# Performance work log

Measured on AMD Instinct MI355X. Metric: run time of the kernel, lower is better.

Reference implementation:

```python
import jax, jax.numpy as jnp
import numpy as np

T, D, F, E, K, R = 16384, 1024, 2048, 8, 2, 16
LORA_SCALING = 2.0


def setup_inputs() -> dict:
    key = jax.random.key(0)
    ks = jax.random.split(key, 9)
    s = 0.02
    return {
        "hidden_states": jax.random.normal(ks[0], (T, D), jnp.float32),
        "gate_weight": jax.random.normal(ks[1], (E, D), jnp.float32) * s,
        "gate_lora_delta": jax.random.normal(ks[2], (E, D), jnp.float32) * s,
        "gate_up_proj": jax.random.normal(ks[3], (E, D, 2 * F), jnp.float32) * s,
        "down_proj": jax.random.normal(ks[4], (E, F, D), jnp.float32) * s,
        "gu_lora_A": jax.random.normal(ks[5], (E, R, D), jnp.float32) * s,
        "gu_lora_B": jax.random.normal(ks[6], (E, 2 * F, R), jnp.float32) * s,
        "dn_lora_A": jax.random.normal(ks[7], (E, R, F), jnp.float32) * s,
        "dn_lora_B": jax.random.normal(ks[8], (E, D, R), jnp.float32) * s,
    }


def reference(hidden_states, gate_weight, gate_lora_delta, gate_up_proj,
              down_proj, gu_lora_A, gu_lora_B, dn_lora_A, dn_lora_B):
    x = hidden_states  # [T, D]
    # --- softmax top-k routing (base gate weight + LoRA delta) ---
    logits = x @ gate_weight.T + x @ gate_lora_delta.T            # [T, E]
    probs = jax.nn.softmax(logits.astype(jnp.float32), axis=-1)   # fp32 softmax
    topk_w, topk_idx = jax.lax.top_k(probs, K)                    # [T, K]
    topk_w = topk_w / jnp.sum(topk_w, axis=-1, keepdims=True)     # norm_topk_prob
    # dense combine weights [T, E]: 0 for unselected experts
    combine = jnp.zeros((x.shape[0], E), jnp.float32)
    combine = combine.at[jnp.arange(x.shape[0])[:, None], topk_idx].set(topk_w)
    # --- per-expert gated MLP with LoRA deltas, masked combine ---
    out = jnp.zeros_like(x, dtype=jnp.float32)
    for e in range(E):  # fixed small expert count
        gu = x @ gate_up_proj[e] + LORA_SCALING * ((x @ gu_lora_A[e].T) @ gu_lora_B[e].T)  # [T, 2F]
        gate, up = jnp.split(gu, 2, axis=-1)
        h = jax.nn.silu(gate) * up                                                        # [T, F]
        y = h @ down_proj[e] + LORA_SCALING * ((h @ dn_lora_A[e].T) @ dn_lora_B[e].T)     # [T, D]
        out = out + combine[:, e:e + 1] * y
    return out.astype(hidden_states.dtype)
```

## Files before the change

kernel.cpp:

```cpp
#include <hip/hip_runtime.h>
#include <stdint.h>

#define T_TOK 16384
#define DH    1024
#define FF    2048
#define NE    8
#define NC    4096
#define PADROWS 33792

typedef __attribute__((ext_vector_type(8))) __bf16 bf16x8;
typedef __attribute__((ext_vector_type(4))) float  f32x4;

__device__ __forceinline__ float bf2f(unsigned short s) {
  unsigned int u = ((unsigned int)s) << 16;
  return __builtin_bit_cast(float, u);
}
__device__ __forceinline__ unsigned short f2bf(float f) {
  unsigned int u = __builtin_bit_cast(unsigned int, f);
  u += 0x7fffu + ((u >> 16) & 1u);
  return (unsigned short)(u >> 16);
}

__device__ __forceinline__ void gload_lds16(const void* g, void* l) {
  __builtin_amdgcn_global_load_lds(
      (__attribute__((address_space(1))) void*)(uintptr_t)g,
      (__attribute__((address_space(3))) void*)(uint32_t)(uintptr_t)l,
      16, 0, 0);
}

__device__ __forceinline__ int origc_gu(int c) {
  int g = c >> 5, wi = c & 31;
  return ((wi >> 4) << 11) | (g * 16 + (wi & 15));
}

__global__ __launch_bounds__(256) void fold_gu_kernel(
    const float* __restrict__ Wg,
    const float* __restrict__ A,
    const float* __restrict__ B,
    unsigned short* __restrict__ Wf)
{
  const int e = blockIdx.x, d0 = blockIdx.y * 64, c0 = blockIdx.z * 64;
  __shared__ float tile[64][65];
  __shared__ float Al[16][64];
  __shared__ float Bl[64][17];
  const int tid = threadIdx.x;
  {
    int r = tid >> 4, dc = (tid & 15) * 4;
    float4 v = *(const float4*)&A[((size_t)e * 16 + r) * DH + d0 + dc];
    Al[r][dc] = v.x; Al[r][dc + 1] = v.y; Al[r][dc + 2] = v.z; Al[r][dc + 3] = v.w;
  }
  {
    int c = tid >> 2, rr = (tid & 3) * 4;
    float4 v = *(const float4*)&B[((size_t)e * NC + origc_gu(c0 + c)) * 16 + rr];
    Bl[c][rr] = v.x; Bl[c][rr + 1] = v.y; Bl[c][rr + 2] = v.z; Bl[c][rr + 3] = v.w;
  }
  __syncthreads();
  const int d = tid >> 2;
  const int cq0 = (tid & 3) * 4;
  float areg[16];
#pragma unroll
  for (int r = 0; r < 16; r++) areg[r] = Al[r][d];
#pragma unroll
  for (int p = 0; p < 4; p++) {
    const int cq = p * 16 + cq0;
    float4 v = *(const float4*)&Wg[((size_t)e * DH + d0 + d) * NC + origc_gu(c0 + cq)];
    float s0 = 0.f, s1 = 0.f, s2 = 0.f, s3 = 0.f;
#pragma unroll
    for (int r = 0; r < 16; r++) {
      float a = areg[r];
      s0 += a * Bl[cq][r];     s1 += a * Bl[cq + 1][r];
      s2 += a * Bl[cq + 2][r]; s3 += a * Bl[cq + 3][r];
    }
    tile[d][cq]     = v.x + 2.f * s0; tile[d][cq + 1] = v.y + 2.f * s1;
    tile[d][cq + 2] = v.z + 2.f * s2; tile[d][cq + 3] = v.w + 2.f * s3;
  }
  __syncthreads();
#pragma unroll
  for (int p = 0; p < 2; p++) {
    int flat = p * 256 + tid;
    int c = flat >> 3, dch = (flat & 7) * 8;
    unsigned short u[8];
#pragma unroll
    for (int j = 0; j < 8; j++) u[j] = f2bf(tile[dch + j][c]);
    *(uint4*)&Wf[((size_t)e * NC + c0 + c) * DH + d0 + dch] = *(uint4*)u;
  }
}

__global__ __launch_bounds__(256) void fold_dn_kernel(
    const float* __restrict__ Wd,
    const float* __restrict__ A,
    const float* __restrict__ B,
    unsigned short* __restrict__ Wf)
{
  const int e = blockIdx.x, f0 = blockIdx.y * 64, d0 = blockIdx.z * 64;
  __shared__ float tile[64][65];
  __shared__ float Al[16][64];
  __shared__ float Bl[64][17];
  const int tid = threadIdx.x;
  {
    int r = tid >> 4, fc = (tid & 15) * 4;
    float4 v = *(const float4*)&A[((size_t)e * 16 + r) * FF + f0 + fc];
    Al[r][fc] = v.x; Al[r][fc + 1] = v.y; Al[r][fc + 2] = v.z; Al[r][fc + 3] = v.w;
  }
  {
    int d = tid >> 2, rr = (tid & 3) * 4;
    float4 v = *(const float4*)&B[((size_t)e * DH + d0 + d) * 16 + rr];
    Bl[d][rr] = v.x; Bl[d][rr + 1] = v.y; Bl[d][rr + 2] = v.z; Bl[d][rr + 3] = v.w;
  }
  __syncthreads();
  const int f = tid >> 2;
  const int dq0 = (tid & 3) * 4;
  float areg[16];
#pragma unroll
  for (int r = 0; r < 16; r++) areg[r] = Al[r][f];
#pragma unroll
  for (int p = 0; p < 4; p++) {
    const int dq = p * 16 + dq0;
    float4 v = *(const float4*)&Wd[((size_t)e * FF + f0 + f) * DH + d0 + dq];
    float s0 = 0.f, s1 = 0.f, s2 = 0.f, s3 = 0.f;
#pragma unroll
    for (int r = 0; r < 16; r++) {
      float a = areg[r];
      s0 += a * Bl[dq][r];     s1 += a * Bl[dq + 1][r];
      s2 += a * Bl[dq + 2][r]; s3 += a * Bl[dq + 3][r];
    }
    tile[f][dq]     = v.x + 2.f * s0; tile[f][dq + 1] = v.y + 2.f * s1;
    tile[f][dq + 2] = v.z + 2.f * s2; tile[f][dq + 3] = v.w + 2.f * s3;
  }
  __syncthreads();
#pragma unroll
  for (int p = 0; p < 2; p++) {
    int flat = p * 256 + tid;
    int d = flat >> 3, fch = (flat & 7) * 8;
    unsigned short u[8];
#pragma unroll
    for (int j = 0; j < 8; j++) u[j] = f2bf(tile[fch + j][d]);
    *(uint4*)&Wf[((size_t)e * DH + d0 + d) * FF + f0 + fch] = *(uint4*)u;
  }
}

__global__ __launch_bounds__(256) void route_kernel(
    const float* __restrict__ X,
    const float* __restrict__ GW,
    const float* __restrict__ GLD,
    unsigned short* __restrict__ Xbf,
    int* __restrict__ tokE, float* __restrict__ tokW, int* __restrict__ counts)
{
  __shared__ float gc[NE * DH];
  __shared__ int bc[NE];
  const int tid = threadIdx.x;
  if (tid < NE) bc[tid] = 0;
  for (int i = tid; i < NE * DH; i += 256) gc[i] = GW[i] + GLD[i];
  __syncthreads();
  const int w = tid >> 6, lane = tid & 63;
  for (int it = 0; it < 8; it++) {
    const int t = blockIdx.x * 32 + w * 8 + it;
    float s[NE];
#pragma unroll
    for (int e = 0; e < NE; e++) s[e] = 0.f;
#pragma unroll
    for (int i = 0; i < 8; i++) {
      const int base = 2 * lane + 128 * i;
      const float2 xv = *(const float2*)&X[(size_t)t * DH + base];
      *(unsigned*)&Xbf[(size_t)t * DH + base] =
          (unsigned)f2bf(xv.x) | ((unsigned)f2bf(xv.y) << 16);
#pragma unroll
      for (int e = 0; e < NE; e++) {
        float2 g2 = *(const float2*)&gc[e * DH + base];
        s[e] += xv.x * g2.x + xv.y * g2.y;
      }
    }
#pragma unroll
    for (int e = 0; e < NE; e++) {
#pragma unroll
      for (int off = 32; off > 0; off >>= 1) s[e] += __shfl_xor(s[e], off);
    }
    int e1 = 0; float l1 = s[0];
#pragma unroll
    for (int e = 1; e < NE; e++) { if (s[e] > l1) { l1 = s[e]; e1 = e; } }
    int e2i = 0; float l2 = -3.4e38f;
#pragma unroll
    for (int e = 0; e < NE; e++) { if (e != e1 && s[e] > l2) { l2 = s[e]; e2i = e; } }
    float r = __expf(l2 - l1);
    float w0 = 1.f / (1.f + r);
    if (lane == 0) {
      tokE[2 * t] = e1; tokE[2 * t + 1] = e2i;
      tokW[2 * t] = w0; tokW[2 * t + 1] = 1.f - w0;
      atomicAdd(&bc[e1], 1); atomicAdd(&bc[e2i], 1);
    }
  }
  __syncthreads();
  if (tid < NE) atomicAdd(&counts[tid], bc[tid]);
}

__global__ void offs_kernel(const int* __restrict__ counts, int* __restrict__ offs) {
  if (threadIdx.x == 0) {
    int run = 0;
#pragma unroll
    for (int e = 0; e < NE; e++) { offs[e] = run; run += (counts[e] + 127) & ~127; }
    offs[NE] = run;
  }
}

__global__ void scatter_kernel(const int* __restrict__ tokE,
                               const int* __restrict__ offs,
                               int* __restrict__ cursor,
                               int* __restrict__ posTok,
                               int* __restrict__ posOf)
{
  const int t = blockIdx.x * 256 + threadIdx.x;
  const int lane = threadIdx.x & 63;
#pragma unroll
  for (int k = 0; k < 2; k++) {
    const int e = tokE[2 * t + k];
    int p = 0;
#pragma unroll
    for (int ei = 0; ei < NE; ei++) {
      unsigned long long mask = __ballot(e == ei);
      if (mask) {
        int leader = __ffsll((unsigned long long)mask) - 1;
        int base = 0;
        if (lane == leader) base = atomicAdd(&cursor[ei], (int)__popcll(mask));
        base = __shfl(base, leader);
        if (e == ei)
          p = offs[ei] + base + (int)__popcll(mask & ((1ull << lane) - 1ull));
      }
    }
    if (p < 0) p = 0;
    if (p >= PADROWS) p = PADROWS - 1;
    posTok[p] = t;
    posOf[2 * t + k] = p;
  }
}

__global__ __launch_bounds__(256) void gemm1_kernel(
    const unsigned short* __restrict__ Xbf,
    const unsigned short* __restrict__ Wgu,
    const int* __restrict__ posTok,
    const int* __restrict__ offs,
    unsigned short* __restrict__ H)
{
  __shared__ __align__(16) unsigned short As[128 * 32];
  __shared__ __align__(16) unsigned short Bs[128 * 32];
  const int n0 = blockIdx.x * 128;
  const int row0 = blockIdx.y * 128;
  if (row0 >= offs[NE]) return;
  int e = 0;
#pragma unroll
  for (int i = 1; i < NE; i++) e += (row0 >= offs[i]) ? 1 : 0;
  const unsigned short* Wb = Wgu + (size_t)e * NC * DH;

  const int tid = threadIdx.x;
  const int lane = tid & 63;
  const int w = tid >> 6;
  const int wm = w >> 1, wn = w & 1;
  const int l15 = lane & 15, quad = lane >> 4;

  const int srow  = tid >> 2;
  const int skoff = (tid & 3) * 8;
  int t0 = posTok[row0 + srow];      if (t0 < 0) t0 = 0;
  int t1 = posTok[row0 + 64 + srow]; if (t1 < 0) t1 = 0;
  const unsigned short* gA0 = Xbf + (size_t)t0 * DH + skoff;
  const unsigned short* gA1 = Xbf + (size_t)t1 * DH + skoff;
  const unsigned short* gB0 = Wb + (size_t)(n0 + srow) * DH + skoff;
  const unsigned short* gB1 = Wb + (size_t)(n0 + 64 + srow) * DH + skoff;
  unsigned short* lA0 = As + (w * 64) * 8;
  unsigned short* lA1 = As + (256 + w * 64) * 8;
  unsigned short* lB0 = Bs + (w * 64) * 8;
  unsigned short* lB1 = Bs + (256 + w * 64) * 8;

  const unsigned short* Ard = As + (size_t)(wm * 64 + l15) * 32 + quad * 8;
  const unsigned short* Brd = Bs + (size_t)(wn * 64 + l15) * 32 + quad * 8;

  f32x4 acc[4][4];
#pragma unroll
  for (int mi = 0; mi < 4; mi++)
#pragma unroll
    for (int ni = 0; ni < 4; ni++) acc[mi][ni] = (f32x4){0.f, 0.f, 0.f, 0.f};

  for (int k0 = 0; k0 < DH; k0 += 32) {
    gload_lds16(gA0, lA0);
    gload_lds16(gA1, lA1);
    gload_lds16(gB0, lB0);
    gload_lds16(gB1, lB1);
    gA0 += 32; gA1 += 32; gB0 += 32; gB1 += 32;
    __syncthreads();
    bf16x8 af[4], bv[4];
#pragma unroll
    for (int mi = 0; mi < 4; mi++) af[mi] = *(const bf16x8*)(Ard + mi * 16 * 32);
#pragma unroll
    for (int ni = 0; ni < 4; ni++) bv[ni] = *(const bf16x8*)(Brd + ni * 16 * 32);
#pragma unroll
    for (int mi = 0; mi < 4; mi++)
#pragma unroll
      for (int ni = 0; ni < 4; ni++)
        acc[mi][ni] = __builtin_amdgcn_mfma_f32_16x16x32_bf16(af[mi], bv[ni], acc[mi][ni], 0, 0, 0);
    __syncthreads();
  }

  const int rowb = row0 + wm * 64;
#pragma unroll
  for (int mi = 0; mi < 4; mi++) {
#pragma unroll
    for (int p = 0; p < 2; p++) {
      f32x4 g = acc[mi][2 * p], u = acc[mi][2 * p + 1];
      int f = (n0 >> 1) + wn * 32 + p * 16 + l15;
#pragma unroll
      for (int r = 0; r < 4; r++) {
        int row = rowb + mi * 16 + quad * 4 + r;
        float gv = g[r];
        float hv = (gv / (1.f + __expf(-gv))) * u[r];
        H[(size_t)row * FF + f] = f2bf(hv);
      }
    }
  }
}

__global__ __launch_bounds__(256) void gemm2_kernel(
    const unsigned short* __restrict__ H,
    const unsigned short* __restrict__ Wdn,
    const int* __restrict__ offs,
    unsigned short* __restrict__ Y)
{
  __shared__ __align__(16) unsigned short As[128 * 32];
  __shared__ __align__(16) unsigned short Bs[128 * 32];
  const int n0 = blockIdx.x * 128;
  const int row0 = blockIdx.y * 128;
  if (row0 >= offs[NE]) return;
  int e = 0;
#pragma unroll
  for (int i = 1; i < NE; i++) e += (row0 >= offs[i]) ? 1 : 0;
  const unsigned short* Wb = Wdn + (size_t)e * DH * FF;

  const int tid = threadIdx.x;
  const int lane = tid & 63;
  const int w = tid >> 6;
  const int wm = w >> 1, wn = w & 1;
  const int l15 = lane & 15, quad = lane >> 4;

  const int srow  = tid >> 2;
  const int skoff = (tid & 3) * 8;
  const unsigned short* gA0 = H + (size_t)(row0 + srow) * FF + skoff;
  const unsigned short* gA1 = H + (size_t)(row0 + 64 + srow) * FF + skoff;
  const unsigned short* gB0 = Wb + (size_t)(n0 + srow) * FF + skoff;
  const unsigned short* gB1 = Wb + (size_t)(n0 + 64 + srow) * FF + skoff;
  unsigned short* lA0 = As + (w * 64) * 8;
  unsigned short* lA1 = As + (256 + w * 64) * 8;
  unsigned short* lB0 = Bs + (w * 64) * 8;
  unsigned short* lB1 = Bs + (256 + w * 64) * 8;

  const unsigned short* Ard = As + (size_t)(wm * 64 + l15) * 32 + quad * 8;
  const unsigned short* Brd = Bs + (size_t)(wn * 64 + l15) * 32 + quad * 8;

  f32x4 acc[4][4];
#pragma unroll
  for (int mi = 0; mi < 4; mi++)
#pragma unroll
    for (int ni = 0; ni < 4; ni++) acc[mi][ni] = (f32x4){0.f, 0.f, 0.f, 0.f};

  for (int k0 = 0; k0 < FF; k0 += 32) {
    gload_lds16(gA0, lA0);
    gload_lds16(gA1, lA1);
    gload_lds16(gB0, lB0);
    gload_lds16(gB1, lB1);
    gA0 += 32; gA1 += 32; gB0 += 32; gB1 += 32;
    __syncthreads();
    bf16x8 af[4], bv[4];
#pragma unroll
    for (int mi = 0; mi < 4; mi++) af[mi] = *(const bf16x8*)(Ard + mi * 16 * 32);
#pragma unroll
    for (int ni = 0; ni < 4; ni++) bv[ni] = *(const bf16x8*)(Brd + ni * 16 * 32);
#pragma unroll
    for (int mi = 0; mi < 4; mi++)
#pragma unroll
      for (int ni = 0; ni < 4; ni++)
        acc[mi][ni] = __builtin_amdgcn_mfma_f32_16x16x32_bf16(af[mi], bv[ni], acc[mi][ni], 0, 0, 0);
    __syncthreads();
  }

#pragma unroll
  for (int mi = 0; mi < 4; mi++)
#pragma unroll
    for (int ni = 0; ni < 4; ni++) {
      int col = n0 + wn * 64 + ni * 16 + l15;
#pragma unroll
      for (int r = 0; r < 4; r++) {
        int row = row0 + wm * 64 + mi * 16 + quad * 4 + r;
        Y[(size_t)row * DH + col] = f2bf(acc[mi][ni][r]);
      }
    }
}

__global__ void combine_kernel(const unsigned short* __restrict__ Y,
                               const int* __restrict__ posOf,
                               const float* __restrict__ tokW,
                               float* __restrict__ out)
{
  int idx = blockIdx.x * 256 + threadIdx.x;
  int t = idx >> 7;
  int c = (idx & 127) * 8;
  int p0 = posOf[2 * t], p1 = posOf[2 * t + 1];
  float w0 = tokW[2 * t], w1 = tokW[2 * t + 1];
  const uint4 a = *(const uint4*)&Y[(size_t)p0 * DH + c];
  const uint4 b = *(const uint4*)&Y[(size_t)p1 * DH + c];
  const unsigned* ap = (const unsigned*)&a;
  const unsigned* bp = (const unsigned*)&b;
  float4 o0, o1;
#pragma unroll
  for (int i = 0; i < 4; i++) {
    float a0 = bf2f((unsigned short)(ap[i] & 0xffff)), a1 = bf2f((unsigned short)(ap[i] >> 16));
    float b0 = bf2f((unsigned short)(bp[i] & 0xffff)), b1 = bf2f((unsigned short)(bp[i] >> 16));
    float r0 = w0 * a0 + w1 * b0;
    float r1 = w0 * a1 + w1 * b1;
    if (i < 2) { ((float*)&o0)[2 * i] = r0; ((float*)&o0)[2 * i + 1] = r1; }
    else       { ((float*)&o1)[2 * (i - 2)] = r0; ((float*)&o1)[2 * (i - 2) + 1] = r1; }
  }
  *(float4*)&out[(size_t)t * DH + c]     = o0;
  *(float4*)&out[(size_t)t * DH + c + 4] = o1;
}

extern "C" void kernel_launch(void* const* d_in, const int* in_sizes, int n_in,
                              void* d_out, int out_size, void* d_ws, size_t ws_size,
                              hipStream_t stream)
{
  const float* X   = (const float*)d_in[0];
  const float* GW  = (const float*)d_in[1];
  const float* GLD = (const float*)d_in[2];
  const float* GUP = (const float*)d_in[3];
  const float* DNP = (const float*)d_in[4];
  const float* GUA = (const float*)d_in[5];
  const float* GUB = (const float*)d_in[6];
  const float* DNA = (const float*)d_in[7];
  const float* DNB = (const float*)d_in[8];
  float* OUT = (float*)d_out;

  char* p = (char*)d_ws;
  unsigned short* Wguf = (unsigned short*)p; p += (size_t)NE * NC * DH * 2;
  unsigned short* Wdnf = (unsigned short*)p; p += (size_t)NE * DH * FF * 2;
  unsigned short* H    = (unsigned short*)p; p += (size_t)PADROWS * FF * 2;
  unsigned short* Y    = (unsigned short*)p; p += (size_t)PADROWS * DH * 2;
  int*   posTok = (int*)p;   p += (size_t)PADROWS * 4;
  int*   posOf  = (int*)p;   p += (size_t)T_TOK * 2 * 4;
  int*   tokE   = (int*)p;   p += (size_t)T_TOK * 2 * 4;
  float* tokW   = (float*)p; p += (size_t)T_TOK * 2 * 4;
  int*   counts = (int*)p;   p += 32;
  int*   cursor = (int*)p;   p += 32;
  int*   offs   = (int*)p;   p += 64;
  if ((size_t)(p - (char*)d_ws) > ws_size) return;

  unsigned short* Xbf = Y;

  hipMemsetAsync(counts, 0, 32 + 32 + 64, stream);
  hipMemsetAsync(posTok, 0xFF, (size_t)PADROWS * 4, stream);

  fold_gu_kernel<<<dim3(NE, DH / 64, NC / 64), 256, 0, stream>>>(GUP, GUA, GUB, Wguf);
  fold_dn_kernel<<<dim3(NE, FF / 64, DH / 64), 256, 0, stream>>>(DNP, DNA, DNB, Wdnf);
  route_kernel<<<T_TOK / 32, 256, 0, stream>>>(X, GW, GLD, Xbf, tokE, tokW, counts);
  offs_kernel<<<1, 64, 0, stream>>>(counts, offs);
  scatter_kernel<<<T_TOK / 256, 256, 0, stream>>>(tokE, offs, cursor, posTok, posOf);
  gemm1_kernel<<<dim3(NC / 128, PADROWS / 128), 256, 0, stream>>>(Xbf, Wguf, posTok, offs, H);
  gemm2_kernel<<<dim3(DH / 128, PADROWS / 128), 256, 0, stream>>>(H, Wdnf, offs, Y);
  combine_kernel<<<(T_TOK * DH / 8) / 256, 256, 0, stream>>>(Y, posOf, tokW, OUT);
}
```

Before: 943.9 us.

## Use 256x256 tiles with 4-stage LDS pipeline and swizzled layout in expert GEMMs

Both grouped GEMMs now use 256x256 output tiles with 512 threads (8 waves, each computing 128x64), padding expert segments to 256 rows. Global-to-LDS loads run in a 4-deep ring, issued three k-steps ahead with explicit vmcnt waits, and the MFMA work is split into two phases separated by barriers and raised wave priority. An XOR swizzle on LDS chunk placement is meant to reduce bank conflicts on fragment reads. The aim is to hide memory latency and raise arithmetic intensity, at the cost of more padding waste, higher register and LDS use, and fewer blocks in flight.

```diff
diff --git a/kernel.cpp b/kernel.cpp
--- a/kernel.cpp
+++ b/kernel.cpp
@@ -6,7 +6,8 @@
 #define FF    2048
 #define NE    8
 #define NC    4096
-#define PADROWS 33792
+#define PADROWS 34816
+#define BK    32
 
 typedef __attribute__((ext_vector_type(8))) __bf16 bf16x8;
 typedef __attribute__((ext_vector_type(4))) float  f32x4;
@@ -34,10 +35,8 @@
 }
 
 __global__ __launch_bounds__(256) void fold_gu_kernel(
-    const float* __restrict__ Wg,
-    const float* __restrict__ A,
-    const float* __restrict__ B,
-    unsigned short* __restrict__ Wf)
+    const float* __restrict__ Wg, const float* __restrict__ A,
+    const float* __restrict__ B, unsigned short* __restrict__ Wf)
 {
   const int e = blockIdx.x, d0 = blockIdx.y * 64, c0 = blockIdx.z * 64;
   __shared__ float tile[64][65];
@@ -87,10 +86,8 @@
 }
 
 __global__ __launch_bounds__(256) void fold_dn_kernel(
-    const float* __restrict__ Wd,
-    const float* __restrict__ A,
-    const float* __restrict__ B,
-    unsigned short* __restrict__ Wf)
+    const float* __restrict__ Wd, const float* __restrict__ A,
+    const float* __restrict__ B, unsigned short* __restrict__ Wf)
 {
   const int e = blockIdx.x, f0 = blockIdx.y * 64, d0 = blockIdx.z * 64;
   __shared__ float tile[64][65];
@@ -197,7 +194,7 @@
   if (threadIdx.x == 0) {
     int run = 0;
 #pragma unroll
-    for (int e = 0; e < NE; e++) { offs[e] = run; run += (counts[e] + 127) & ~127; }
+    for (int e = 0; e < NE; e++) { offs[e] = run; run += (counts[e] + 255) & ~255; }
     offs[NE] = run;
   }
 }
@@ -233,17 +230,35 @@
   }
 }
 
-__global__ __launch_bounds__(256) void gemm1_kernel(
+
+#define STAGE_A(s) { unsigned short* d_ = (unsigned short*)&lds[(s) & 3][0][w * 512]; \
+  gload_lds16(gA0 + (size_t)(s) * BK, d_); gload_lds16(gA1 + (size_t)(s) * BK, d_ + 4096); }
+#define STAGE_B(s) { unsigned short* d_ = (unsigned short*)&lds[(s) & 3][1][w * 512]; \
+  gload_lds16(gB0 + (size_t)(s) * BK, d_); gload_lds16(gB1 + (size_t)(s) * BK, d_ + 4096); }
+
+#define PHASE_MFMA(ACCROW, AV)                                              \
+  __builtin_amdgcn_s_barrier();                                             \
+  __builtin_amdgcn_s_setprio(1);                                            \
+  _Pragma("unroll")                                                         \
+  for (int mi = 0; mi < 4; mi++)                                            \
+    _Pragma("unroll")                                                       \
+    for (int ni = 0; ni < 4; ni++)                                          \
+      acc[(ACCROW) + mi][ni] = __builtin_amdgcn_mfma_f32_16x16x32_bf16(     \
+          AV[mi], b[ni], acc[(ACCROW) + mi][ni], 0, 0, 0);                  \
+  __builtin_amdgcn_s_setprio(0);                                            \
+  __builtin_amdgcn_s_barrier();
+
+__global__ __launch_bounds__(512, 2) void gemm1_kernel(
     const unsigned short* __restrict__ Xbf,
     const unsigned short* __restrict__ Wgu,
     const int* __restrict__ posTok,
     const int* __restrict__ offs,
     unsigned short* __restrict__ H)
 {
-  __shared__ __align__(16) unsigned short As[128 * 32];
-  __shared__ __align__(16) unsigned short Bs[128 * 32];
-  const int n0 = blockIdx.x * 128;
-  const int row0 = blockIdx.y * 128;
+  __shared__ __align__(16) unsigned short lds[4][2][8192];
+  const int NT = DH / BK;
+  const int n0 = blockIdx.x * 256;
+  const int row0 = blockIdx.y * 256;
   if (row0 >= offs[NE]) return;
   int e = 0;
 #pragma unroll
@@ -253,54 +268,57 @@
   const int tid = threadIdx.x;
   const int lane = tid & 63;
   const int w = tid >> 6;
-  const int wm = w >> 1, wn = w & 1;
+  const int wm = w >> 2, wn = w & 3;
   const int l15 = lane & 15, quad = lane >> 4;
 
-  const int srow  = tid >> 2;
-  const int skoff = (tid & 3) * 8;
-  int t0 = posTok[row0 + srow];      if (t0 < 0) t0 = 0;
-  int t1 = posTok[row0 + 64 + srow]; if (t1 < 0) t1 = 0;
-  const unsigned short* gA0 = Xbf + (size_t)t0 * DH + skoff;
-  const unsigned short* gA1 = Xbf + (size_t)t1 * DH + skoff;
-  const unsigned short* gB0 = Wb + (size_t)(n0 + srow) * DH + skoff;
-  const unsigned short* gB1 = Wb + (size_t)(n0 + 64 + srow) * DH + skoff;
-  unsigned short* lA0 = As + (w * 64) * 8;
-  unsigned short* lA1 = As + (256 + w * 64) * 8;
-  unsigned short* lB0 = Bs + (w * 64) * 8;
-  unsigned short* lB1 = Bs + (256 + w * 64) * 8;
-
-  const unsigned short* Ard = As + (size_t)(wm * 64 + l15) * 32 + quad * 8;
-  const unsigned short* Brd = Bs + (size_t)(wn * 64 + l15) * 32 + quad * 8;
-
-  f32x4 acc[4][4];
-#pragma unroll
-  for (int mi = 0; mi < 4; mi++)
+  const int srow = tid >> 2;
+  const int sch  = (tid & 3) ^ ((srow >> 1) & 3);
+  int t0 = posTok[row0 + srow];       if (t0 < 0) t0 = 0;
+  int t1 = posTok[row0 + 128 + srow]; if (t1 < 0) t1 = 0;
+  const unsigned short* gA0 = Xbf + (size_t)t0 * DH + sch * 8;
+  const unsigned short* gA1 = Xbf + (size_t)t1 * DH + sch * 8;
+  const unsigned short* gB0 = Wb + (size_t)(n0 + srow) * DH + sch * 8;
+  const unsigned short* gB1 = Wb + (size_t)(n0 + 128 + srow) * DH + sch * 8;
+
+  const int slot  = quad ^ ((l15 >> 1) & 3);
+  const int aBase = (wm * 128 + l15) * 32 + slot * 8;
+  const int bBase = (wn * 64 + l15) * 32 + slot * 8;
+
+  f32x4 acc[8][4];
+#pragma unroll
+  for (int mi = 0; mi < 8; mi++)
 #pragma unroll
     for (int ni = 0; ni < 4; ni++) acc[mi][ni] = (f32x4){0.f, 0.f, 0.f, 0.f};
 
-  for (int k0 = 0; k0 < DH; k0 += 32) {
-    gload_lds16(gA0, lA0);
-    gload_lds16(gA1, lA1);
-    gload_lds16(gB0, lB0);
-    gload_lds16(gB1, lB1);
-    gA0 += 32; gA1 += 32; gB0 += 32; gB1 += 32;
-    __syncthreads();
-    bf16x8 af[4], bv[4];
-#pragma unroll
-    for (int mi = 0; mi < 4; mi++) af[mi] = *(const bf16x8*)(Ard + mi * 16 * 32);
-#pragma unroll
-    for (int ni = 0; ni < 4; ni++) bv[ni] = *(const bf16x8*)(Brd + ni * 16 * 32);
-#pragma unroll
-    for (int mi = 0; mi < 4; mi++)
-#pragma unroll
-      for (int ni = 0; ni < 4; ni++)
-        acc[mi][ni] = __builtin_amdgcn_mfma_f32_16x16x32_bf16(af[mi], bv[ni], acc[mi][ni], 0, 0, 0);
-    __syncthreads();
-  }
-
-  const int rowb = row0 + wm * 64;
-#pragma unroll
-  for (int mi = 0; mi < 4; mi++) {
+  STAGE_A(0); STAGE_B(0);
+  STAGE_A(1); STAGE_B(1);
+  STAGE_A(2); STAGE_B(2);
+  asm volatile("s_waitcnt vmcnt(8)" ::: "memory");
+  __builtin_amdgcn_s_barrier();
+
+  for (int kt = 0; kt < NT; ++kt) {
+    const unsigned short* LA = &lds[kt & 3][0][0];
+    const unsigned short* LB = &lds[kt & 3][1][0];
+    bf16x8 a[4], b[4];
+#pragma unroll
+    for (int i = 0; i < 4; i++) a[i] = *(const bf16x8*)&LA[aBase + i * 512];
+#pragma unroll
+    for (int i = 0; i < 4; i++) b[i] = *(const bf16x8*)&LB[bBase + i * 512];
+    if (kt + 3 < NT) STAGE_A(kt + 3);
+    PHASE_MFMA(0, a)
+    bf16x8 a2[4];
+#pragma unroll
+    for (int i = 0; i < 4; i++) a2[i] = *(const bf16x8*)&LA[aBase + (4 + i) * 512];
+    if (kt + 3 < NT) STAGE_B(kt + 3);
+    if (kt + 3 < NT)       { asm volatile("s_waitcnt vmcnt(8)" ::: "memory"); }
+    else if (kt + 3 == NT) { asm volatile("s_waitcnt vmcnt(4)" ::: "memory"); }
+    else if (kt + 1 < NT)  { asm volatile("s_waitcnt vmcnt(0)" ::: "memory"); }
+    PHASE_MFMA(4, a2)
+  }
+
+  const int rowb = row0 + wm * 128;
+#pragma unroll
+  for (int mi = 0; mi < 8; mi++) {
 #pragma unroll
     for (int p = 0; p < 2; p++) {
       f32x4 g = acc[mi][2 * p], u = acc[mi][2 * p + 1];
@@ -316,16 +334,16 @@
   }
 }
 
-__global__ __launch_bounds__(256) void gemm2_kernel(
+__global__ __launch_bounds__(512, 2) void gemm2_kernel(
     const unsigned short* __restrict__ H,
     const unsigned short* __restrict__ Wdn,
     const int* __restrict__ offs,
     unsigned short* __restrict__ Y)
 {
-  __shared__ __align__(16) unsigned short As[128 * 32];
-  __shared__ __align__(16) unsigned short Bs[128 * 32];
-  const int n0 = blockIdx.x * 128;
-  const int row0 = blockIdx.y * 128;
+  __shared__ __align__(16) unsigned short lds[4][2][8192];
+  const int NT = FF / BK;
+  const int n0 = blockIdx.x * 256;
+  const int row0 = blockIdx.y * 256;
   if (row0 >= offs[NE]) return;
   int e = 0;
 #pragma unroll
@@ -335,57 +353,60 @@
   const int tid = threadIdx.x;
   const int lane = tid & 63;
   const int w = tid >> 6;
-  const int wm = w >> 1, wn = w & 1;
+  const int wm = w >> 2, wn = w & 3;
   const int l15 = lane & 15, quad = lane >> 4;
 
-  const int srow  = tid >> 2;
-  const int skoff = (tid & 3) * 8;
-  const unsigned short* gA0 = H + (size_t)(row0 + srow) * FF + skoff;
-  const unsigned short* gA1 = H + (size_t)(row0 + 64 + srow) * FF + skoff;
-  const unsigned short* gB0 = Wb + (size_t)(n0 + srow) * FF + skoff;
-  const unsigned short* gB1 = Wb + (size_t)(n0 + 64 + srow) * FF + skoff;
-  unsigned short* lA0 = As + (w * 64) * 8;
-  unsigned short* lA1 = As + (256 + w * 64) * 8;
-  unsigned short* lB0 = Bs + (w * 64) * 8;
-  unsigned short* lB1 = Bs + (256 + w * 64) * 8;
-
-  const unsigned short* Ard = As + (size_t)(wm * 64 + l15) * 32 + quad * 8;
-  const unsigned short* Brd = Bs + (size_t)(wn * 64 + l15) * 32 + quad * 8;
-
-  f32x4 acc[4][4];
-#pragma unroll
-  for (int mi = 0; mi < 4; mi++)
+  const int srow = tid >> 2;
+  const int sch  = (tid & 3) ^ ((srow >> 1) & 3);
+  const unsigned short* gA0 = H + (size_t)(row0 + srow) * FF + sch * 8;
+  const unsigned short* gA1 = H + (size_t)(row0 + 128 + srow) * FF + sch * 8;
+  const unsigned short* gB0 = Wb + (size_t)(n0 + srow) * FF + sch * 8;
+  const unsigned short* gB1 = Wb + (size_t)(n0 + 128 + srow) * FF + sch * 8;
+
+  const int slot  = quad ^ ((l15 >> 1) & 3);
+  const int aBase = (wm * 128 + l15) * 32 + slot * 8;
+  const int bBase = (wn * 64 + l15) * 32 + slot * 8;
+
+  f32x4 acc[8][4];
+#pragma unroll
+  for (int mi = 0; mi < 8; mi++)
 #pragma unroll
     for (int ni = 0; ni < 4; ni++) acc[mi][ni] = (f32x4){0.f, 0.f, 0.f, 0.f};
 
-  for (int k0 = 0; k0 < FF; k0 += 32) {
-    gload_lds16(gA0, lA0);
-    gload_lds16(gA1, lA1);
-    gload_lds16(gB0, lB0);
-    gload_lds16(gB1, lB1);
-    gA0 += 32; gA1 += 32; gB0 += 32; gB1 += 32;
-    __syncthreads();
-    bf16x8 af[4], bv[4];
-#pragma unroll
-    for (int mi = 0; mi < 4; mi++) af[mi] = *(const bf16x8*)(Ard + mi * 16 * 32);
-#pragma unroll
-    for (int ni = 0; ni < 4; ni++) bv[ni] = *(const bf16x8*)(Brd + ni * 16 * 32);
-#pragma unroll
-    for (int mi = 0; mi < 4; mi++)
-#pragma unroll
-      for (int ni = 0; ni < 4; ni++)
-        acc[mi][ni] = __builtin_amdgcn_mfma_f32_16x16x32_bf16(af[mi], bv[ni], acc[mi][ni], 0, 0, 0);
-    __syncthreads();
-  }
-
-#pragma unroll
-  for (int mi = 0; mi < 4; mi++)
+  STAGE_A(0); STAGE_B(0);
+  STAGE_A(1); STAGE_B(1);
+  STAGE_A(2); STAGE_B(2);
+  asm volatile("s_waitcnt vmcnt(8)" ::: "memory");
+  __builtin_amdgcn_s_barrier();
+
+  for (int kt = 0; kt < NT; ++kt) {
+    const unsigned short* LA = &lds[kt & 3][0][0];
+    const unsigned short* LB = &lds[kt & 3][1][0];
+    bf16x8 a[4], b[4];
+#pragma unroll
+    for (int i = 0; i < 4; i++) a[i] = *(const bf16x8*)&LA[aBase + i * 512];
+#pragma unroll
+    for (int i = 0; i < 4; i++) b[i] = *(const bf16x8*)&LB[bBase + i * 512];
+    if (kt + 3 < NT) STAGE_A(kt + 3);
+    PHASE_MFMA(0, a)
+    bf16x8 a2[4];
+#pragma unroll
+    for (int i = 0; i < 4; i++) a2[i] = *(const bf16x8*)&LA[aBase + (4 + i) * 512];
+    if (kt + 3 < NT) STAGE_B(kt + 3);
+    if (kt + 3 < NT)       { asm volatile("s_waitcnt vmcnt(8)" ::: "memory"); }
+    else if (kt + 3 == NT) { asm volatile("s_waitcnt vmcnt(4)" ::: "memory"); }
+    else if (kt + 1 < NT)  { asm volatile("s_waitcnt vmcnt(0)" ::: "memory"); }
+    PHASE_MFMA(4, a2)
+  }
+
+#pragma unroll
+  for (int mi = 0; mi < 8; mi++)
 #pragma unroll
     for (int ni = 0; ni < 4; ni++) {
       int col = n0 + wn * 64 + ni * 16 + l15;
 #pragma unroll
       for (int r = 0; r < 4; r++) {
-        int row = row0 + wm * 64 + mi * 16 + quad * 4 + r;
+        int row = row0 + wm * 128 + mi * 16 + quad * 4 + r;
         Y[(size_t)row * DH + col] = f2bf(acc[mi][ni][r]);
       }
     }
@@ -458,7 +479,7 @@
   route_kernel<<<T_TOK / 32, 256, 0, stream>>>(X, GW, GLD, Xbf, tokE, tokW, counts);
   offs_kernel<<<1, 64, 0, stream>>>(counts, offs);
   scatter_kernel<<<T_TOK / 256, 256, 0, stream>>>(tokE, offs, cursor, posTok, posOf);
-  gemm1_kernel<<<dim3(NC / 128, PADROWS / 128), 256, 0, stream>>>(Xbf, Wguf, posTok, offs, H);
-  gemm2_kernel<<<dim3(DH / 128, PADROWS / 128), 256, 0, stream>>>(H, Wdnf, offs, Y);
+  gemm1_kernel<<<dim3(NC / 256, PADROWS / 256), 512, 0, stream>>>(Xbf, Wguf, posTok, offs, H);
+  gemm2_kernel<<<dim3(DH / 256, PADROWS / 256), 512, 0, stream>>>(H, Wdnf, offs, Y);
   combine_kernel<<<(T_TOK * DH / 8) / 256, 256, 0, stream>>>(Y, posOf, tokW, OUT);
 }
```

Measured after the change: 925.4 us. No clear change (-2.0%).
